# Performance work log

Hardware: AMD Instinct MI355X
Metric: run time of the kernel (lower is better)

The kernel has to match this reference:

```python
import jax, jax.numpy as jnp
import numpy as np
from jax import lax

TIMESTEPS = 10
KSIZE = 2
STRIDE = 2


def setup_inputs() -> dict:
    key = jax.random.key(0)
    k1, _ = jax.random.split(key)
    x = jax.random.normal(k1, (32, 96, 128, 128), dtype=jnp.float32)
    # torch init: np.full((1, C, 1, 1), 0.1)
    pool_strength = jnp.ones((1, 96, 1, 1), dtype=jnp.float32) * 0.1
    return {"x": x, "pool_strength": pool_strength}


def _maxpool3x3_same(x):
    # MaxPool2d(kernel=3, stride=1, padding=1) on NCHW
    return lax.reduce_window(
        x, -jnp.inf, lax.max,
        window_dimensions=(1, 1, 3, 3),
        window_strides=(1, 1, 1, 1),
        padding=((0, 0), (0, 0), (1, 1), (1, 1)))


def reference(x, pool_strength):
    def step(cur, _):
        pooled = _maxpool3x3_same(cur)
        cur = cur + pool_strength * (pooled - cur)
        return cur, None

    cur, _ = lax.scan(step, x, None, length=TIMESTEPS)
    # AvgPool2d(kernel=2, stride=2, padding=0)
    s = lax.reduce_window(
        cur, 0.0, lax.add,
        window_dimensions=(1, 1, KSIZE, KSIZE),
        window_strides=(1, 1, STRIDE, STRIDE),
        padding='VALID')
    return s / float(KSIZE * KSIZE)
```

## Files before the change

kernel.cpp:

```cpp
#include <hip/hip_runtime.h>


#define TSTEPS 10
#define PW 128
#define HP 132
#define HROWS 31

__device__ __forceinline__ float dpp_left(float x) {
    int r = __builtin_amdgcn_update_dpp((int)0xff800000, __float_as_int(x),
                                        0x111, 0xf, 0xf, false);
    return __int_as_float(r);
}
__device__ __forceinline__ float dpp_right(float x) {
    int r = __builtin_amdgcn_update_dpp((int)0xff800000, __float_as_int(x),
                                        0x101, 0xf, 0xf, false);
    return __int_as_float(r);
}

__device__ __forceinline__ float max3f(float a, float b, float c) {
    return fmaxf(fmaxf(a, b), c);
}

__device__ __forceinline__ void hmax_row(const float* v, float* h) {
    float vl = dpp_left(v[7]);
    float vr = dpp_right(v[0]);
    h[0] = max3f(vl, v[0], v[1]);
#pragma unroll
    for (int c = 1; c < 7; ++c) h[c] = max3f(v[c - 1], v[c], v[c + 1]);
    h[7] = max3f(v[6], v[7], vr);
}

__device__ __forceinline__ void ld8(const float* a, float* d) {
    float4 u = ((const float4*)a)[0], v = ((const float4*)a)[1];
    d[0] = u.x; d[1] = u.y; d[2] = u.z; d[3] = u.w;
    d[4] = v.x; d[5] = v.y; d[6] = v.z; d[7] = v.w;
}
__device__ __forceinline__ void st8(float* a, const float* d) {
    ((float4*)a)[0] = make_float4(d[0], d[1], d[2], d[3]);
    ((float4*)a)[1] = make_float4(d[4], d[5], d[6], d[7]);
}

__device__ __forceinline__ void do_step(float cur[4][8], float p, int tx, int ty,
                                        float* __restrict__ topBuf,
                                        float* __restrict__ botBuf) {
    const float NEG = -__builtin_huge_valf();
    const int x0 = tx * 8;

    float h0[8], h3[8];
    hmax_row(cur[0], h0);
    hmax_row(cur[3], h3);
    if (ty > 0)     st8(topBuf + (ty - 1) * HP + x0, h0);
    if (ty < HROWS) st8(botBuf + ty * HP + x0, h3);

    __syncthreads();

    float hm[8], hnx[8];
    if (ty > 0) {
        ld8(botBuf + (ty - 1) * HP + x0, hm);
    } else {
#pragma unroll
        for (int c = 0; c < 8; ++c) hm[c] = NEG;
    }
    if (ty < HROWS) {
        ld8(topBuf + ty * HP + x0, hnx);
    } else {
#pragma unroll
        for (int c = 0; c < 8; ++c) hnx[c] = NEG;
    }

    float h1[8], h2[8];
    hmax_row(cur[1], h1);
    hmax_row(cur[2], h2);
#pragma unroll
    for (int c = 0; c < 8; ++c) {
        float v = max3f(h0[c], h1[c], h2[c]);
        cur[1][c] = fmaf(p, v - cur[1][c], cur[1][c]);
    }
#pragma unroll
    for (int c = 0; c < 8; ++c) {
        float v = max3f(h1[c], h2[c], h3[c]);
        cur[2][c] = fmaf(p, v - cur[2][c], cur[2][c]);
    }

#pragma unroll
    for (int c = 0; c < 8; ++c) {
        float v = max3f(hm[c], h0[c], h1[c]);
        cur[0][c] = fmaf(p, v - cur[0][c], cur[0][c]);
    }
#pragma unroll
    for (int c = 0; c < 8; ++c) {
        float v = max3f(h2[c], h3[c], hnx[c]);
        cur[3][c] = fmaf(p, v - cur[3][c], cur[3][c]);
    }
}

__global__ __launch_bounds__(512, 4)
void cpool_kernel(const float* __restrict__ x, const float* __restrict__ ps,
                  float* __restrict__ out) {
    __shared__ float lds[2][2][HROWS * HP];

    const int b = blockIdx.x;
    const float p = ps[b % 96];

    const int tx = threadIdx.x & 15;
    const int ty = threadIdx.x >> 4;
    const int x0 = tx * 8;
    const int y0 = ty * 4;

    const float* __restrict__ xp = x + (size_t)b * (PW * PW);

    float cur[4][8];
#pragma unroll
    for (int r = 0; r < 4; ++r) ld8(xp + (y0 + r) * PW + x0, cur[r]);

#pragma unroll 1
    for (int tt = 0; tt < TSTEPS / 2; ++tt) {
        do_step(cur, p, tx, ty, lds[0][0], lds[0][1]);
        do_step(cur, p, tx, ty, lds[1][0], lds[1][1]);
    }

    float* __restrict__ op = out + (size_t)b * (64 * 64);
#pragma unroll
    for (int r2 = 0; r2 < 2; ++r2) {
        float4 o;
        o.x = 0.25f * (cur[2*r2][0] + cur[2*r2][1] + cur[2*r2+1][0] + cur[2*r2+1][1]);
        o.y = 0.25f * (cur[2*r2][2] + cur[2*r2][3] + cur[2*r2+1][2] + cur[2*r2+1][3]);
        o.z = 0.25f * (cur[2*r2][4] + cur[2*r2][5] + cur[2*r2+1][4] + cur[2*r2+1][5]);
        o.w = 0.25f * (cur[2*r2][6] + cur[2*r2][7] + cur[2*r2+1][6] + cur[2*r2+1][7]);
        *(float4*)(op + (size_t)((2 * ty + r2) * 64 + tx * 4)) = o;
    }
}

extern "C" void kernel_launch(void* const* d_in, const int* in_sizes, int n_in,
                              void* d_out, int out_size, void* d_ws, size_t ws_size,
                              hipStream_t stream) {
    const float* x  = (const float*)d_in[0];
    const float* ps = (const float*)d_in[1];
    float* out = (float*)d_out;
    (void)in_sizes; (void)n_in; (void)out_size; (void)d_ws; (void)ws_size;

    cpool_kernel<<<dim3(32 * 96), dim3(512), 0, stream>>>(x, ps, out);
}
```

Baseline: 291.0 us.

## Remap to wave-per-16-row strips and fuse two timesteps per barrier

Each wavefront now owns a 16-row strip with each lane holding two adjacent columns, so horizontal neighbours come from wave-wide DPP shifts (row_shr/row_shl by one lane) instead of per-thread column blocks. Two timesteps are computed per LDS exchange and barrier by exchanging two halo rows and recomputing the boundary rows redundantly. This halves synchronisation and shrinks shared memory, at the cost of extra halo recomputation and more complex boundary handling. The DPP control values (0x138/0x130) need to be correct wave shifts for the edge columns to be right.

```diff
diff --git a/kernel.cpp b/kernel.cpp
--- a/kernel.cpp
+++ b/kernel.cpp
@@ -3,17 +3,15 @@
 
 #define TSTEPS 10
 #define PW 128
-#define HP 132
-#define HROWS 31
 
-__device__ __forceinline__ float dpp_left(float x) {
+__device__ __forceinline__ float wshr1(float x) {
     int r = __builtin_amdgcn_update_dpp((int)0xff800000, __float_as_int(x),
-                                        0x111, 0xf, 0xf, false);
+                                        0x138, 0xf, 0xf, false);
     return __int_as_float(r);
 }
-__device__ __forceinline__ float dpp_right(float x) {
+__device__ __forceinline__ float wshl1(float x) {
     int r = __builtin_amdgcn_update_dpp((int)0xff800000, __float_as_int(x),
-                                        0x101, 0xf, 0xf, false);
+                                        0x130, 0xf, 0xf, false);
     return __int_as_float(r);
 }
 
@@ -21,113 +19,124 @@
     return fmaxf(fmaxf(a, b), c);
 }
 
-__device__ __forceinline__ void hmax_row(const float* v, float* h) {
-    float vl = dpp_left(v[7]);
-    float vr = dpp_right(v[0]);
-    h[0] = max3f(vl, v[0], v[1]);
-#pragma unroll
-    for (int c = 1; c < 7; ++c) h[c] = max3f(v[c - 1], v[c], v[c + 1]);
-    h[7] = max3f(v[6], v[7], vr);
+__device__ __forceinline__ void hmax2(float a, float b, float& h0, float& h1) {
+    float L = wshr1(b);
+    float R = wshl1(a);
+    h0 = max3f(L, a, b);
+    h1 = max3f(a, b, R);
 }
 
-__device__ __forceinline__ void ld8(const float* a, float* d) {
-    float4 u = ((const float4*)a)[0], v = ((const float4*)a)[1];
-    d[0] = u.x; d[1] = u.y; d[2] = u.z; d[3] = u.w;
-    d[4] = v.x; d[5] = v.y; d[6] = v.z; d[7] = v.w;
-}
-__device__ __forceinline__ void st8(float* a, const float* d) {
-    ((float4*)a)[0] = make_float4(d[0], d[1], d[2], d[3]);
-    ((float4*)a)[1] = make_float4(d[4], d[5], d[6], d[7]);
-}
+__device__ __forceinline__ void round2(float c[16][2], float p, int w, int lane,
+                                       float4* __restrict__ bufA,
+                                       float4* __restrict__ bufB) {
+    const float NEG = -__builtin_huge_valf();
 
-__device__ __forceinline__ void do_step(float cur[4][8], float p, int tx, int ty,
-                                        float* __restrict__ topBuf,
-                                        float* __restrict__ botBuf) {
-    const float NEG = -__builtin_huge_valf();
-    const int x0 = tx * 8;
-
-    float h0[8], h3[8];
-    hmax_row(cur[0], h0);
-    hmax_row(cur[3], h3);
-    if (ty > 0)     st8(topBuf + (ty - 1) * HP + x0, h0);
-    if (ty < HROWS) st8(botBuf + ty * HP + x0, h3);
-
+    bufA[(w << 6) + lane] = make_float4(c[14][0], c[14][1], c[15][0], c[15][1]);
+    bufB[(w << 6) + lane] = make_float4(c[0][0],  c[0][1],  c[1][0],  c[1][1]);
     __syncthreads();
 
-    float hm[8], hnx[8];
-    if (ty > 0) {
-        ld8(botBuf + (ty - 1) * HP + x0, hm);
-    } else {
+    float m2a=NEG,m2b=NEG,m1a=NEG,m1b=NEG,p0a=NEG,p0b=NEG,p1a=NEG,p1b=NEG;
+    if (w > 0) { float4 t = bufA[((w-1) << 6) + lane]; m2a=t.x; m2b=t.y; m1a=t.z; m1b=t.w; }
+    if (w < 7) { float4 t = bufB[((w+1) << 6) + lane]; p0a=t.x; p0b=t.y; p1a=t.z; p1b=t.w; }
+
+    float h0m0,h0m1, h0c0,h0c1, h0n0,h0n1;
+    hmax2(c[0][0], c[0][1], h0m0, h0m1);
+    hmax2(c[1][0], c[1][1], h0c0, h0c1);
+
+    float h1m0,h1m1, h1c0,h1c1, h1n0,h1n1;
+
+    hmax2(c[2][0], c[2][1], h0n0, h0n1);
+    float s1a = fmaf(p, max3f(h0m0,h0c0,h0n0) - c[1][0], c[1][0]);
+    float s1b = fmaf(p, max3f(h0m1,h0c1,h0n1) - c[1][1], c[1][1]);
+    hmax2(s1a, s1b, h1m0, h1m1);
+    float h1_1a = h1m0, h1_1b = h1m1;
+    h0m0=h0c0; h0m1=h0c1; h0c0=h0n0; h0c1=h0n1;
+
+    hmax2(c[3][0], c[3][1], h0n0, h0n1);
+    float sAa = fmaf(p, max3f(h0m0,h0c0,h0n0) - c[2][0], c[2][0]);
+    float sAb = fmaf(p, max3f(h0m1,h0c1,h0n1) - c[2][1], c[2][1]);
+    hmax2(sAa, sAb, h1c0, h1c1);
+    float h1_2a = h1c0, h1_2b = h1c1;
+    h0m0=h0c0; h0m1=h0c1; h0c0=h0n0; h0c1=h0n1;
+
 #pragma unroll
-        for (int c = 0; c < 8; ++c) hm[c] = NEG;
-    }
-    if (ty < HROWS) {
-        ld8(topBuf + ty * HP + x0, hnx);
-    } else {
-#pragma unroll
-        for (int c = 0; c < 8; ++c) hnx[c] = NEG;
+    for (int j = 3; j <= 14; ++j) {
+        hmax2(c[j+1][0], c[j+1][1], h0n0, h0n1);
+        float sa = fmaf(p, max3f(h0m0,h0c0,h0n0) - c[j][0], c[j][0]);
+        float sb = fmaf(p, max3f(h0m1,h0c1,h0n1) - c[j][1], c[j][1]);
+        hmax2(sa, sb, h1n0, h1n1);
+        c[j-1][0] = fmaf(p, max3f(h1m0,h1c0,h1n0) - sAa, sAa);
+        c[j-1][1] = fmaf(p, max3f(h1m1,h1c1,h1n1) - sAb, sAb);
+        sAa = sa; sAb = sb;
+        h1m0=h1c0; h1m1=h1c1; h1c0=h1n0; h1c1=h1n1;
+        h0m0=h0c0; h0m1=h0c1; h0c0=h0n0; h0c1=h0n1;
     }
 
-    float h1[8], h2[8];
-    hmax_row(cur[1], h1);
-    hmax_row(cur[2], h2);
-#pragma unroll
-    for (int c = 0; c < 8; ++c) {
-        float v = max3f(h0[c], h1[c], h2[c]);
-        cur[1][c] = fmaf(p, v - cur[1][c], cur[1][c]);
-    }
-#pragma unroll
-    for (int c = 0; c < 8; ++c) {
-        float v = max3f(h1[c], h2[c], h3[c]);
-        cur[2][c] = fmaf(p, v - cur[2][c], cur[2][c]);
-    }
+    hmax2(p0a, p0b, h0n0, h0n1);
+    float s15a = fmaf(p, max3f(h0m0,h0c0,h0n0) - c[15][0], c[15][0]);
+    float s15b = fmaf(p, max3f(h0m1,h0c1,h0n1) - c[15][1], c[15][1]);
+    hmax2(s15a, s15b, h1n0, h1n1);
+    c[14][0] = fmaf(p, max3f(h1m0,h1c0,h1n0) - sAa, sAa);
+    c[14][1] = fmaf(p, max3f(h1m1,h1c1,h1n1) - sAb, sAb);
+    h0m0=h0c0; h0m1=h0c1; h0c0=h0n0; h0c1=h0n1;
+    hmax2(p1a, p1b, h0n0, h0n1);
+    float s16a = fmaf(p, max3f(h0m0,h0c0,h0n0) - p0a, p0a);
+    float s16b = fmaf(p, max3f(h0m1,h0c1,h0n1) - p0b, p0b);
+    if (w == 7) { s16a = NEG; s16b = NEG; }
+    float h1x0, h1x1;
+    hmax2(s16a, s16b, h1x0, h1x1);
+    c[15][0] = fmaf(p, max3f(h1c0, h1n0, h1x0) - s15a, s15a);
+    c[15][1] = fmaf(p, max3f(h1c1, h1n1, h1x1) - s15b, s15b);
 
-#pragma unroll
-    for (int c = 0; c < 8; ++c) {
-        float v = max3f(hm[c], h0[c], h1[c]);
-        cur[0][c] = fmaf(p, v - cur[0][c], cur[0][c]);
-    }
-#pragma unroll
-    for (int c = 0; c < 8; ++c) {
-        float v = max3f(h2[c], h3[c], hnx[c]);
-        cur[3][c] = fmaf(p, v - cur[3][c], cur[3][c]);
-    }
+    float hA0,hA1, hB0,hB1, hC0,hC1, hD0,hD1;
+    hmax2(m2a, m2b, hA0, hA1);
+    hmax2(m1a, m1b, hB0, hB1);
+    hmax2(c[0][0], c[0][1], hC0, hC1);
+    hmax2(c[1][0], c[1][1], hD0, hD1);
+    float sm1a = fmaf(p, max3f(hA0,hB0,hC0) - m1a, m1a);
+    float sm1b = fmaf(p, max3f(hA1,hB1,hC1) - m1b, m1b);
+    if (w == 0) { sm1a = NEG; sm1b = NEG; }
+    float s0a = fmaf(p, max3f(hB0,hC0,hD0) - c[0][0], c[0][0]);
+    float s0b = fmaf(p, max3f(hB1,hC1,hD1) - c[0][1], c[0][1]);
+    hmax2(sm1a, sm1b, hA0, hA1);
+    hmax2(s0a,  s0b,  hB0, hB1);
+    c[0][0] = fmaf(p, max3f(hA0, hB0, h1_1a) - s0a, s0a);
+    c[0][1] = fmaf(p, max3f(hA1, hB1, h1_1b) - s0b, s0b);
+    c[1][0] = fmaf(p, max3f(hB0, h1_1a, h1_2a) - s1a, s1a);
+    c[1][1] = fmaf(p, max3f(hB1, h1_1b, h1_2b) - s1b, s1b);
 }
 
 __global__ __launch_bounds__(512, 4)
 void cpool_kernel(const float* __restrict__ x, const float* __restrict__ ps,
                   float* __restrict__ out) {
-    __shared__ float lds[2][2][HROWS * HP];
+    __shared__ float4 lds[2][2][8][64];
 
     const int b = blockIdx.x;
     const float p = ps[b % 96];
 
-    const int tx = threadIdx.x & 15;
-    const int ty = threadIdx.x >> 4;
-    const int x0 = tx * 8;
-    const int y0 = ty * 4;
+    const int w    = threadIdx.x >> 6;
+    const int lane = threadIdx.x & 63;
 
-    const float* __restrict__ xp = x + (size_t)b * (PW * PW);
+    const float2* __restrict__ xp2 =
+        (const float2*)(x + (size_t)b * (PW * PW));
 
-    float cur[4][8];
+    float c[16][2];
 #pragma unroll
-    for (int r = 0; r < 4; ++r) ld8(xp + (y0 + r) * PW + x0, cur[r]);
+    for (int r = 0; r < 16; ++r) {
+        float2 t = xp2[(w * 16 + r) * 64 + lane];
+        c[r][0] = t.x; c[r][1] = t.y;
+    }
 
 #pragma unroll 1
-    for (int tt = 0; tt < TSTEPS / 2; ++tt) {
-        do_step(cur, p, tx, ty, lds[0][0], lds[0][1]);
-        do_step(cur, p, tx, ty, lds[1][0], lds[1][1]);
+    for (int t = 0; t < TSTEPS / 2; ++t) {
+        round2(c, p, w, lane, &lds[t & 1][0][0][0], &lds[t & 1][1][0][0]);
     }
 
     float* __restrict__ op = out + (size_t)b * (64 * 64);
 #pragma unroll
-    for (int r2 = 0; r2 < 2; ++r2) {
-        float4 o;
-        o.x = 0.25f * (cur[2*r2][0] + cur[2*r2][1] + cur[2*r2+1][0] + cur[2*r2+1][1]);
-        o.y = 0.25f * (cur[2*r2][2] + cur[2*r2][3] + cur[2*r2+1][2] + cur[2*r2+1][3]);
-        o.z = 0.25f * (cur[2*r2][4] + cur[2*r2][5] + cur[2*r2+1][4] + cur[2*r2+1][5]);
-        o.w = 0.25f * (cur[2*r2][6] + cur[2*r2][7] + cur[2*r2+1][6] + cur[2*r2+1][7]);
-        *(float4*)(op + (size_t)((2 * ty + r2) * 64 + tx * 4)) = o;
+    for (int i = 0; i < 8; ++i) {
+        float o = 0.25f * (c[2*i][0] + c[2*i][1] + c[2*i+1][0] + c[2*i+1][1]);
+        op[(size_t)((w * 8 + i) * 64 + lane)] = o;
     }
 }
 
```

Result: slower. 297.0 us (+2.1%).

## Replace LDS-synchronized time stepping with wave-level streaming row pipeline

Applied to the files above, without the earlier changes.

Each wave now handles half of a 128x128 plane and streams rows top to bottom. All ten time steps run as a register-resident stage pipeline, with a 10-row halo recomputed at the split. Horizontal neighbours come from wave-wide DPP row shifts, which removes the LDS buffers and all __syncthreads. The cost is redundant halo computation and a serial per-row dependency chain, with row loads prefetched a few rows ahead.

```diff
diff --git a/kernel.cpp b/kernel.cpp
--- a/kernel.cpp
+++ b/kernel.cpp
@@ -1,133 +1,102 @@
 #include <hip/hip_runtime.h>
 
 
-#define TSTEPS 10
 #define PW 128
-#define HP 132
-#define HROWS 31
+#define NSTAGE 10
+#define HALO 10
+#define CORE 64
+#define NITER 84
+#define UNROLL 3
+#define SENT -1.0e37f
 
-__device__ __forceinline__ float dpp_left(float x) {
+__device__ __forceinline__ float wshr1(float x) {
     int r = __builtin_amdgcn_update_dpp((int)0xff800000, __float_as_int(x),
-                                        0x111, 0xf, 0xf, false);
+                                        0x138, 0xf, 0xf, false);
     return __int_as_float(r);
 }
-__device__ __forceinline__ float dpp_right(float x) {
+__device__ __forceinline__ float wshl1(float x) {
     int r = __builtin_amdgcn_update_dpp((int)0xff800000, __float_as_int(x),
-                                        0x101, 0xf, 0xf, false);
+                                        0x130, 0xf, 0xf, false);
     return __int_as_float(r);
 }
-
 __device__ __forceinline__ float max3f(float a, float b, float c) {
     return fmaxf(fmaxf(a, b), c);
 }
 
-__device__ __forceinline__ void hmax_row(const float* v, float* h) {
-    float vl = dpp_left(v[7]);
-    float vr = dpp_right(v[0]);
-    h[0] = max3f(vl, v[0], v[1]);
+__global__ __attribute__((amdgpu_flat_work_group_size(256, 256),
+                          amdgpu_waves_per_eu(4, 5)))
+void cpool_kernel(const float* __restrict__ x, const float* __restrict__ ps,
+                  float* __restrict__ out) {
+    const int wv    = threadIdx.x >> 6;
+    const int lane  = threadIdx.x & 63;
+    const int wg    = blockIdx.x * 4 + wv;
+    const int plane = wg >> 1;
+    const int rbase = (wg & 1) * CORE;
+    const float p = ps[plane % 96];
+
+    const float2* __restrict__ xp = (const float2*)(x + (size_t)plane * (PW * PW));
+    float* __restrict__ op = out + (size_t)plane * (64 * 64) + lane;
+
+    float H[3][NSTAGE][2];
+    float S[NSTAGE][2];
 #pragma unroll
-    for (int c = 1; c < 7; ++c) h[c] = max3f(v[c - 1], v[c], v[c + 1]);
-    h[7] = max3f(v[6], v[7], vr);
-}
-
-__device__ __forceinline__ void ld8(const float* a, float* d) {
-    float4 u = ((const float4*)a)[0], v = ((const float4*)a)[1];
-    d[0] = u.x; d[1] = u.y; d[2] = u.z; d[3] = u.w;
-    d[4] = v.x; d[5] = v.y; d[6] = v.z; d[7] = v.w;
-}
-__device__ __forceinline__ void st8(float* a, const float* d) {
-    ((float4*)a)[0] = make_float4(d[0], d[1], d[2], d[3]);
-    ((float4*)a)[1] = make_float4(d[4], d[5], d[6], d[7]);
-}
-
-__device__ __forceinline__ void do_step(float cur[4][8], float p, int tx, int ty,
-                                        float* __restrict__ topBuf,
-                                        float* __restrict__ botBuf) {
-    const float NEG = -__builtin_huge_valf();
-    const int x0 = tx * 8;
-
-    float h0[8], h3[8];
-    hmax_row(cur[0], h0);
-    hmax_row(cur[3], h3);
-    if (ty > 0)     st8(topBuf + (ty - 1) * HP + x0, h0);
-    if (ty < HROWS) st8(botBuf + ty * HP + x0, h3);
-
-    __syncthreads();
-
-    float hm[8], hnx[8];
-    if (ty > 0) {
-        ld8(botBuf + (ty - 1) * HP + x0, hm);
-    } else {
+    for (int i = 0; i < NSTAGE; ++i) {
+        S[i][0] = SENT; S[i][1] = SENT;
 #pragma unroll
-        for (int c = 0; c < 8; ++c) hm[c] = NEG;
-    }
-    if (ty < HROWS) {
-        ld8(topBuf + ty * HP + x0, hnx);
-    } else {
-#pragma unroll
-        for (int c = 0; c < 8; ++c) hnx[c] = NEG;
+        for (int k = 0; k < 3; ++k) { H[k][i][0] = SENT; H[k][i][1] = SENT; }
     }
 
-    float h1[8], h2[8];
-    hmax_row(cur[1], h1);
-    hmax_row(cur[2], h2);
+    const int t0 = rbase - HALO;
+    float2 raw[UNROLL];
 #pragma unroll
-    for (int c = 0; c < 8; ++c) {
-        float v = max3f(h0[c], h1[c], h2[c]);
-        cur[1][c] = fmaf(p, v - cur[1][c], cur[1][c]);
-    }
-#pragma unroll
-    for (int c = 0; c < 8; ++c) {
-        float v = max3f(h1[c], h2[c], h3[c]);
-        cur[2][c] = fmaf(p, v - cur[2][c], cur[2][c]);
+    for (int k = 0; k < UNROLL; ++k) {
+        int tr = t0 + k;
+        raw[k] = ((unsigned)tr < (unsigned)PW) ? xp[tr * 64 + lane]
+                                               : make_float2(SENT, SENT);
     }
 
-#pragma unroll
-    for (int c = 0; c < 8; ++c) {
-        float v = max3f(hm[c], h0[c], h1[c]);
-        cur[0][c] = fmaf(p, v - cur[0][c], cur[0][c]);
-    }
-#pragma unroll
-    for (int c = 0; c < 8; ++c) {
-        float v = max3f(h2[c], h3[c], hnx[c]);
-        cur[3][c] = fmaf(p, v - cur[3][c], cur[3][c]);
-    }
-}
-
-__global__ __launch_bounds__(512, 4)
-void cpool_kernel(const float* __restrict__ x, const float* __restrict__ ps,
-                  float* __restrict__ out) {
-    __shared__ float lds[2][2][HROWS * HP];
-
-    const int b = blockIdx.x;
-    const float p = ps[b % 96];
-
-    const int tx = threadIdx.x & 15;
-    const int ty = threadIdx.x >> 4;
-    const int x0 = tx * 8;
-    const int y0 = ty * 4;
-
-    const float* __restrict__ xp = x + (size_t)b * (PW * PW);
-
-    float cur[4][8];
-#pragma unroll
-    for (int r = 0; r < 4; ++r) ld8(xp + (y0 + r) * PW + x0, cur[r]);
+    float pend = 0.0f;
 
 #pragma unroll 1
-    for (int tt = 0; tt < TSTEPS / 2; ++tt) {
-        do_step(cur, p, tx, ty, lds[0][0], lds[0][1]);
-        do_step(cur, p, tx, ty, lds[1][0], lds[1][1]);
-    }
+    for (int tb = 0; tb < NITER; tb += UNROLL) {
+#pragma unroll
+        for (int u = 0; u < UNROLL; ++u) {
+            const int t = t0 + tb + u;
+            float c0 = raw[u].x, c1 = raw[u].y;
 
-    float* __restrict__ op = out + (size_t)b * (64 * 64);
+            {
+                int tn = t + UNROLL;
+                raw[u] = ((unsigned)tn < (unsigned)PW)
+                             ? xp[tn * 64 + lane]
+                             : make_float2(SENT, SENT);
+            }
+
 #pragma unroll
-    for (int r2 = 0; r2 < 2; ++r2) {
-        float4 o;
-        o.x = 0.25f * (cur[2*r2][0] + cur[2*r2][1] + cur[2*r2+1][0] + cur[2*r2+1][1]);
-        o.y = 0.25f * (cur[2*r2][2] + cur[2*r2][3] + cur[2*r2+1][2] + cur[2*r2+1][3]);
-        o.z = 0.25f * (cur[2*r2][4] + cur[2*r2][5] + cur[2*r2+1][4] + cur[2*r2+1][5]);
-        o.w = 0.25f * (cur[2*r2][6] + cur[2*r2][7] + cur[2*r2+1][6] + cur[2*r2+1][7]);
-        *(float4*)(op + (size_t)((2 * ty + r2) * 64 + tx * 4)) = o;
+            for (int i = 0; i < NSTAGE; ++i) {
+                float L = wshr1(c1);
+                float R = wshl1(c0);
+                float hn0 = max3f(L, c0, c1);
+                float hn1 = max3f(c0, c1, R);
+                float o0 = fmaf(p, max3f(H[u % 3][i][0], H[(u + 1) % 3][i][0], hn0)
+                                       - S[i][0], S[i][0]);
+                float o1 = fmaf(p, max3f(H[u % 3][i][1], H[(u + 1) % 3][i][1], hn1)
+                                       - S[i][1], S[i][1]);
+                H[(u + 2) % 3][i][0] = hn0;
+                H[(u + 2) % 3][i][1] = hn1;
+                S[i][0] = c0; S[i][1] = c1;
+                c0 = o0; c1 = o1;
+            }
+
+            const int rr = t - NSTAGE;
+            if (rr >= rbase && rr < rbase + CORE) {
+                float hs = c0 + c1;
+                if ((rr & 1) == 0) {
+                    pend = hs;
+                } else {
+                    op[(rr >> 1) * 64] = 0.25f * (pend + hs);
+                }
+            }
+        }
     }
 }
 
@@ -139,5 +108,5 @@
     float* out = (float*)d_out;
     (void)in_sizes; (void)n_in; (void)out_size; (void)d_ws; (void)ws_size;
 
-    cpool_kernel<<<dim3(32 * 96), dim3(512), 0, stream>>>(x, ps, out);
+    cpool_kernel<<<dim3(1536), dim3(256), 0, stream>>>(x, ps, out);
 }
```

After: 311.5 us. 7.0% more time.
